# Kernel optimization log

Measured on AMD Instinct MI355X. Metric: run time of the kernel, lower is better.

The kernel has to match this reference:

```python
import jax, jax.numpy as jnp
import numpy as np

EPS = 1e-5
NEG = jnp.float32(-1e30)
SPP_LEVEL = 3
SPATIAL_SCALE = 0.125


def conv2d(x, w, b, pad):
    out = jax.lax.conv_general_dilated(x, w, (1, 1), [(pad, pad), (pad, pad)],
                                       dimension_numbers=('NCHW', 'OIHW', 'NCHW'))
    return out + b[None, :, None, None]


def bn2d(x, g, b):  # BatchNorm2d, training-mode batch stats (biased var), as in torch forward
    m = x.mean((0, 2, 3), keepdims=True)
    v = x.var((0, 2, 3), keepdims=True)
    return (x - m) * jax.lax.rsqrt(v + EPS) * g[None, :, None, None] + b[None, :, None, None]


def bn1d(x, g, b):
    m = x.mean(0)
    v = x.var(0)
    return (x - m) * jax.lax.rsqrt(v + EPS) * g + b


def maxpool2(x):
    return jax.lax.reduce_window(x, -jnp.inf, jax.lax.max, (1, 1, 2, 2), (1, 1, 2, 2), 'VALID')


def roi_spp(feat, roi):
    # feat: (B,C,Hf,Wf); roi: (R,5) int [im,x1,y1,x2,y2] in input-image coords.
    im = roi[:, 0].astype(jnp.int32)
    s = (roi[:, 1:].astype(jnp.float32) * SPATIAL_SCALE).astype(jnp.int32)  # trunc, coords >= 0
    c1, r1, c2, r2 = s[:, 0], s[:, 1], s[:, 2], s[:, 3]
    R = roi.shape[0]
    Hf, Wf = feat.shape[2], feat.shape[3]
    rows = jnp.arange(Hf)
    cols = jnp.arange(Wf)
    rmask = (rows[None, :] >= r1[:, None]) & (rows[None, :] <= r2[:, None])  # (R,Hf)
    w = c2 - c1 + 1
    froi = feat[im]  # (R,C,Hf,Wf)
    pieces = []
    for l in range(1, SPP_LEVEL + 1):  # adaptive_max_pool2d to (1,l) per level
        k = jnp.arange(l)
        lo = c1[:, None] + (k[None, :] * w[:, None]) // l
        hi = c1[:, None] + ((k[None, :] + 1) * w[:, None] + l - 1) // l - 1
        cmask = (cols[None, None, :] >= lo[:, :, None]) & (cols[None, None, :] <= hi[:, :, None])  # (R,l,Wf)
        mask = rmask[:, None, :, None] & cmask[:, :, None, :]  # (R,l,Hf,Wf)
        vals = jnp.where(mask[:, None], froi[:, :, None], NEG)  # (R,C,l,Hf,Wf)
        pieces.append(vals.max((-2, -1)).reshape(R, -1))  # channel-major flatten, like torch .view
    return jnp.concatenate(pieces, axis=1)  # (R, C*(1+2+3)) = (R, 3072)


def _forward(x, phocTensor, roi,
             c1w, c1b, g1, b1, c2w, c2b, g2, b2, c3w, c3b, g3, b3,
             c4w, c4b, g4, b4, c5w, c5b, g5, b5,
             f1w, f1b, g6, b6, f2w, f2b, g7, b7):
    out = jnp.pad(x, ((0, 0), (0, 0), (2, 2), (2, 2)), mode='edge')  # replicate pad
    out = maxpool2(jax.nn.relu(bn2d(conv2d(out, c1w, c1b, 0), g1, b1)))
    out = maxpool2(jax.nn.relu(bn2d(conv2d(out, c2w, c2b, 2), g2, b2)))
    out = jax.nn.relu(bn2d(conv2d(out, c3w, c3b, 1), g3, b3))
    out = maxpool2(jax.nn.relu(bn2d(conv2d(out, c4w, c4b, 1), g4, b4)))
    out = jax.nn.relu(bn2d(conv2d(out, c5w, c5b, 1), g5, b5))  # (B,512,6,16)
    out = roi_spp(out, roi)  # (R,3072)
    out = jax.nn.relu(bn1d(out @ f1w.T + f1b, g6, b6))
    out = jnp.concatenate([out, phocTensor], axis=1)  # (R, 2048+5853)
    out = jax.nn.relu(bn1d(out @ f2w.T + f2b, g7, b7))
    return out


def setup_inputs() -> dict:
    key = jax.random.key(0)
    ks = jax.random.split(key, 24)
    B, R = 64, 256
    x = jax.random.normal(ks[0], (B, 1, 48, 128), jnp.float32)
    # ROIs [im, x1, y1, x2, y2], guaranteed non-empty after /8 scaling
    im = jax.random.randint(ks[1], (R,), 0, B)
    x1 = jax.random.randint(ks[2], (R,), 0, 64)
    x2 = jnp.minimum(x1 + jax.random.randint(ks[3], (R,), 32, 64), 127)
    y1 = jax.random.randint(ks[4], (R,), 0, 16)
    y2 = jnp.minimum(y1 + jax.random.randint(ks[5], (R,), 16, 32), 47)
    roi = jnp.stack([im, x1, y1, x2, y2], axis=1).astype(jnp.int32)
    phocTensor = jax.random.uniform(ks[6], (R, 5853), jnp.float32)

    def he(k, shape):
        fan_in = int(np.prod(shape[1:]))
        return jax.random.normal(k, shape, jnp.float32) * np.sqrt(2.0 / fan_in).astype(np.float32)

    d = {'x': x, 'roi': roi, 'phocTensor': phocTensor}
    conv_shapes = [('c1', (64, 1, 5, 5)), ('c2', (128, 64, 5, 5)), ('c3', (256, 128, 3, 3)),
                   ('c4', (512, 256, 3, 3)), ('c5', (512, 512, 3, 3))]
    for i, (nm, sh) in enumerate(conv_shapes):
        d[nm + 'w'] = he(ks[7 + i], sh)
        d[nm + 'b'] = jnp.zeros((sh[0],), jnp.float32)
        d['g' + str(i + 1)] = jnp.ones((sh[0],), jnp.float32)
        d['b' + str(i + 1)] = jnp.zeros((sh[0],), jnp.float32)
    d['f1w'] = he(ks[12], (2048, 3072)); d['f1b'] = jnp.zeros((2048,), jnp.float32)
    d['g6'] = jnp.ones((2048,), jnp.float32); d['b6'] = jnp.zeros((2048,), jnp.float32)
    d['f2w'] = he(ks[13], (2048, 2048 + 5853)); d['f2b'] = jnp.zeros((2048,), jnp.float32)
    d['g7'] = jnp.ones((2048,), jnp.float32); d['b7'] = jnp.zeros((2048,), jnp.float32)
    return d


def reference(x, roi, phocTensor,
              c1w, c1b, g1, b1, c2w, c2b, g2, b2, c3w, c3b, g3, b3,
              c4w, c4b, g4, b4, c5w, c5b, g5, b5,
              f1w, f1b, g6, b6, f2w, f2b, g7, b7):
    return _forward(x, phocTensor, roi,
                    c1w, c1b, g1, b1, c2w, c2b, g2, b2, c3w, c3b, g3, b3,
                    c4w, c4b, g4, b4, c5w, c5b, g5, b5,
                    f1w, f1b, g6, b6, f2w, f2b, g7, b7)
```

## Files before the change

kernel.cpp:

```cpp
#include <hip/hip_runtime.h>
#include <hip/hip_bf16.h>


typedef __bf16 bf16;
using bf16x4 = __attribute__((ext_vector_type(4))) __bf16;
using bf16x8 = __attribute__((ext_vector_type(8))) __bf16;
using f32x4  = __attribute__((ext_vector_type(4))) float;

__device__ __forceinline__ void split2(float v, bf16& h, bf16& l) {
  bf16 hb = (bf16)v;
  h = hb;
  l = (bf16)(v - (float)hb);
}

__device__ __forceinline__ int iclamp(int v, int lo, int hi) {
  return v < lo ? lo : (v > hi ? hi : v);
}

__device__ __forceinline__ void gld_lds16(const bf16* g, void* lds) {
  __builtin_amdgcn_global_load_lds(
      (const __attribute__((address_space(1))) unsigned int*)g,
      (__attribute__((address_space(3))) unsigned int*)lds, 16, 0, 0);
}

__device__ __forceinline__ void wconv_tx(const float* __restrict__ w,
                                         bf16* __restrict__ oh_,
                                         bf16* __restrict__ ol_,
                                         int CI, int KS, int i, int total) {
  if (i >= total) return;
  int ci = i % CI; int t = i / CI; int kw = t % KS; t /= KS; int kh = t % KS; int co = t / KS;
  float v = w[(((size_t)co * CI + ci) * KS + kh) * KS + kw];
  bf16 h, l; split2(v, h, l);
  oh_[i] = h;
  if (ol_) ol_[i] = l;
}

__global__ __launch_bounds__(256) void prep_k(const float* __restrict__ c2w,
                                              const float* __restrict__ c3w,
                                              const float* __restrict__ c4w,
                                              const float* __restrict__ c5w,
                                              const float* __restrict__ f1w,
                                              const float* __restrict__ f2w,
                                              const float* __restrict__ phoc,
                                              bf16* __restrict__ Wc2h,
                                              bf16* __restrict__ Wc3h,
                                              bf16* __restrict__ Wc4h,
                                              bf16* __restrict__ Wc5h,
                                              bf16* __restrict__ Wc5l,
                                              bf16* __restrict__ Wf1,
                                              bf16* __restrict__ Wf2,
                                              bf16* __restrict__ cch,
                                              bf16* __restrict__ ccl) {
  int b = blockIdx.x;
  int tid = threadIdx.x;
  if (b < 800)  { wconv_tx(c2w, Wc2h, nullptr, 64, 5, b * 256 + tid, 204800); return; }
  b -= 800;
  if (b < 1152) { wconv_tx(c3w, Wc3h, nullptr, 128, 3, b * 256 + tid, 294912); return; }
  b -= 1152;
  if (b < 4608) { wconv_tx(c4w, Wc4h, nullptr, 256, 3, b * 256 + tid, 1179648); return; }
  b -= 4608;
  if (b < 9216) { wconv_tx(c5w, Wc5h, Wc5l, 512, 3, b * 256 + tid, 2359296); return; }
  b -= 9216;
  if (b < 6144) {
    int i = b * 256 + tid;
    const float4 v = *(const float4*)(f1w + (size_t)i * 4);
    bf16x4 o = { (bf16)v.x, (bf16)v.y, (bf16)v.z, (bf16)v.w };
    *(bf16x4*)(Wf1 + (size_t)i * 4) = o;
    return;
  }
  b -= 6144;
  if (b < 16384) {
    int i = b * 256 + tid;
    int k = (i & 2047) * 4, n = i >> 11;
    const float* xp = f2w + (size_t)n * 7901 + k;
    bf16x4 o;
#pragma unroll
    for (int j = 0; j < 4; j++) o[j] = (bf16)((k + j < 7901) ? xp[j] : 0.f);
    *(bf16x4*)(Wf2 + (size_t)n * 8192 + k) = o;
    return;
  }
  b -= 16384;
  {
    int i = b * 256 + tid;
    if (i >= 256 * 6144) return;
    int k = i % 6144, r = i / 6144;
    int col = 2048 + k;
    float v = (col < 7901) ? phoc[(size_t)r * 5853 + (col - 2048)] : 0.f;
    bf16 h, l; split2(v, h, l);
    cch[(size_t)r * 8192 + col] = h;
    ccl[(size_t)r * 8192 + col] = l;
  }
}

__global__ __launch_bounds__(256) void conv1_stats_k(const float* __restrict__ x,
                                                     const float* __restrict__ wt,
                                                     float* __restrict__ part) {
  int co0 = blockIdx.y * 8;
  float sums[8] = {0.f}, sqs[8] = {0.f};
  for (int r = 0; r < 16; r++) {
    int pix = blockIdx.x * 4096 + r * 256 + threadIdx.x;
    int w = pix & 127; int t = pix >> 7; int h = t % 48; int n = t / 48;
    const float* ip = x + (size_t)n * 48 * 128;
    int ihs[5], iws[5];
#pragma unroll
    for (int k = 0; k < 5; k++) {
      ihs[k] = iclamp(h + k - 2, 0, 47);
      iws[k] = iclamp(w + k - 2, 0, 127);
    }
    float win[25];
#pragma unroll
    for (int kh = 0; kh < 5; kh++)
#pragma unroll
      for (int kw = 0; kw < 5; kw++) win[kh * 5 + kw] = ip[ihs[kh] * 128 + iws[kw]];
#pragma unroll
    for (int j = 0; j < 8; j++) {
      const float* wp = wt + (size_t)(co0 + j) * 25;
      float acc = 0.f;
#pragma unroll
      for (int k = 0; k < 25; k++) acc += win[k] * wp[k];
      sums[j] += acc; sqs[j] += acc * acc;
    }
  }
  __shared__ float ls[256], lq[256];
  for (int j = 0; j < 8; j++) {
    ls[threadIdx.x] = sums[j]; lq[threadIdx.x] = sqs[j];
    __syncthreads();
    for (int o = 128; o > 0; o >>= 1) {
      if (threadIdx.x < o) { ls[threadIdx.x] += ls[threadIdx.x + o]; lq[threadIdx.x] += lq[threadIdx.x + o]; }
      __syncthreads();
    }
    if (threadIdx.x == 0) {
      int c = co0 + j;
      part[((size_t)c * 96 + blockIdx.x) * 2 + 0] = ls[0];
      part[((size_t)c * 96 + blockIdx.x) * 2 + 1] = lq[0];
    }
    __syncthreads();
  }
}

__global__ __launch_bounds__(256) void conv1_apply_k(const float* __restrict__ x,
                                                     const float* __restrict__ wt,
                                                     const float* __restrict__ scale,
                                                     const float* __restrict__ shift,
                                                     bf16* __restrict__ yh,
                                                     bf16* __restrict__ yl) {
  int i = blockIdx.x * 256 + threadIdx.x;
  if (i >= 64 * 28 * 68) return;
  int owp = i % 68; int t = i / 68; int ohp = t % 28; int n = t / 28;
  int co0 = blockIdx.y * 8;
  int oh = ohp - 2, ow = owp - 2;
  bf16x8 hv, lv;
#pragma unroll
  for (int j = 0; j < 8; j++) { hv[j] = (bf16)0.f; lv[j] = (bf16)0.f; }
  if (oh >= 0 && oh < 24 && ow >= 0 && ow < 64) {
    const float* ip = x + (size_t)n * 48 * 128;
    int shr[6], swc[6];
#pragma unroll
    for (int k = 0; k < 6; k++) {
      shr[k] = iclamp(2 * oh + k - 2, 0, 47);
      swc[k] = iclamp(2 * ow + k - 2, 0, 127);
    }
    float win[36];
#pragma unroll
    for (int r = 0; r < 6; r++)
#pragma unroll
      for (int c = 0; c < 6; c++) win[r * 6 + c] = ip[shr[r] * 128 + swc[c]];
#pragma unroll
    for (int j = 0; j < 8; j++) {
      const float* wp = wt + (size_t)(co0 + j) * 25;
      float sc = scale[co0 + j], sh = shift[co0 + j];
      float m = -1e30f;
#pragma unroll
      for (int dy = 0; dy < 2; dy++)
#pragma unroll
        for (int dx = 0; dx < 2; dx++) {
          float acc = 0.f;
#pragma unroll
          for (int kh = 0; kh < 5; kh++)
#pragma unroll
            for (int kw = 0; kw < 5; kw++)
              acc += win[(kh + dy) * 6 + kw + dx] * wp[kh * 5 + kw];
          m = fmaxf(m, acc * sc + sh);
        }
      float v = fmaxf(m, 0.f);
      bf16 h, l; split2(v, h, l);
      hv[j] = h; lv[j] = l;
    }
  }
  size_t o = (size_t)i * 64 + co0;
  *(bf16x8*)(yh + o) = hv;
  *(bf16x8*)(yl + o) = lv;
}

__global__ __launch_bounds__(256) void conv2_gemm_k(const bf16* __restrict__ Ahi,
                                                    const bf16* __restrict__ Bhi,
                                                    float* __restrict__ Cout,
                                                    float* __restrict__ part) {
  __shared__ bf16 Ash[416 * 64];
  __shared__ bf16 Bsh[128 * 64];
  __shared__ float red[2][128][8];
  const int t = threadIdx.x;
  const int lane = t & 63, w = t >> 6;
  const int m0 = blockIdx.x * 128;
  const int img = m0 / 1536;
  const int oh0 = (m0 % 1536) >> 6;
  const size_t abase = ((size_t)(img * 28 + oh0) * 68) * 64;

#pragma unroll
  for (int i = 0; i < 13; i++) {
    int f = i * 256 + t;
    int p = f >> 3; if (p > 407) p = 407;
    int s = f & 7;
    int ss = s ^ (p & 7);
    gld_lds16(Ahi + abase + (size_t)p * 64 + ss * 8,
              (char*)Ash + (size_t)(i * 256 + w * 64) * 16);
  }

  size_t boff[4];
#pragma unroll
  for (int i = 0; i < 4; i++) {
    int f = (i * 4 + w) * 64 + lane;
    int row = f >> 3, slot = f & 7;
    int ss = slot ^ (row & 7);
    boff[i] = (size_t)row * 1600 + ss * 8;
  }

  const int wrow = w >> 1, wcol = w & 1;
  const int kg = lane >> 4, l15 = lane & 15;
  int pixb[4];
#pragma unroll
  for (int q = 0; q < 4; q++) pixb[q] = wrow * 68 + q * 16 + l15;
  int brb[4], bmk[4];
#pragma unroll
  for (int q = 0; q < 4; q++) {
    int rb = wcol * 64 + q * 16 + l15;
    brb[q] = rb * 128; bmk[q] = rb & 7;
  }
  const char* Ashb = (const char*)Ash;
  const char* Bshb = (const char*)Bsh;

  f32x4 acc[4][4] = {};
  for (int kc = 0; kc < 25; ++kc) {
    const int kh = kc / 5, kw = kc % 5;
    const int kofs = kh * 68 + kw;
    const int k0 = kc * 64;
#pragma unroll
    for (int i = 0; i < 4; i++)
      gld_lds16(Bhi + boff[i] + k0, (char*)Bsh + (i * 4 + w) * 1024);
    __syncthreads();
#pragma unroll
    for (int ks = 0; ks < 2; ks++) {
      const int slot = ks * 4 + kg;
      bf16x8 ah[4], bh[4];
#pragma unroll
      for (int q = 0; q < 4; q++) {
        int pix = pixb[q] + kofs;
        ah[q] = *(const bf16x8*)(Ashb + pix * 128 + ((slot ^ (pix & 7)) << 4));
        bh[q] = *(const bf16x8*)(Bshb + brb[q] + ((slot ^ bmk[q]) << 4));
      }
#pragma unroll
      for (int mi = 0; mi < 4; mi++)
#pragma unroll
        for (int ni = 0; ni < 4; ni++)
          acc[mi][ni] = __builtin_amdgcn_mfma_f32_16x16x32_bf16(ah[mi], bh[ni], acc[mi][ni], 0, 0, 0);
    }
    __syncthreads();
  }

  const int crow0 = kg * 4, ccol = l15;
#pragma unroll
  for (int mi = 0; mi < 4; mi++) {
    int m = m0 + wrow * 64 + mi * 16 + crow0;
#pragma unroll
    for (int ni = 0; ni < 4; ni++) {
      int nn = wcol * 64 + ni * 16 + ccol;
      float* cp = Cout + (size_t)m * 128 + nn;
#pragma unroll
      for (int jj = 0; jj < 4; jj++) cp[(size_t)jj * 128] = acc[mi][ni][jj];
    }
  }
  const int contrib = kg * 2 + wrow;
#pragma unroll
  for (int ni = 0; ni < 4; ni++) {
    float s = 0.f, q = 0.f;
#pragma unroll
    for (int mi = 0; mi < 4; mi++)
#pragma unroll
      for (int jj = 0; jj < 4; jj++) {
        float v = acc[mi][ni][jj];
        s += v; q += v * v;
      }
    int coll = wcol * 64 + ni * 16 + ccol;
    red[0][coll][contrib] = s;
    red[1][coll][contrib] = q;
  }
  __syncthreads();
  if (t < 128) {
    float s = 0.f, q = 0.f;
#pragma unroll
    for (int j = 0; j < 8; j++) { s += red[0][t][j]; q += red[1][t][j]; }
    size_t c = t;
    part[(c * gridDim.x + blockIdx.x) * 2 + 0] = s;
    part[(c * gridDim.x + blockIdx.x) * 2 + 1] = q;
  }
}

template<int CI, int KS, int OH, int OW, int CO, bool ALO, bool BLO, int SPLIT>
__global__ __launch_bounds__(256) void conv_gemm_k(const bf16* __restrict__ Ahi,
                                                   const bf16* __restrict__ Alo,
                                                   const bf16* __restrict__ Bhi,
                                                   const bf16* __restrict__ Blo,
                                                   float* __restrict__ Cout,
                                                   float* __restrict__ part) {
  static_assert(CI % 64 == 0, "chunk must not straddle ci segments");
  constexpr int K = KS * KS * CI;
  constexpr int IWP = OW + KS - 1;
  constexpr int NCH = K / 64;
  static_assert(NCH % SPLIT == 0, "split must divide chunk count");
  constexpr int NCHS = NCH / SPLIT;
  constexpr int M = 64 * OH * OW;
  __shared__ bf16 Ash[128 * 64];
  __shared__ bf16 Asl[ALO ? 128 * 64 : 64];
  __shared__ bf16 Bsh[128 * 64];
  __shared__ bf16 Bsl[BLO ? 128 * 64 : 64];
  __shared__ float red[2][128][8];
  const int t = threadIdx.x;
  const int lane = t & 63, w = t >> 6;
  const int m0 = blockIdx.x * 128, n0 = blockIdx.y * 128;
  const int z = (SPLIT > 1) ? blockIdx.z : 0;

  int apix[4]; size_t boff[4];
#pragma unroll
  for (int i = 0; i < 4; i++) {
    int f = (i * 4 + w) * 64 + lane;
    int row = f >> 3, slot = f & 7;
    int ss = slot ^ (row & 7);
    int m = m0 + row;
    int n = m / (OH * OW); int rem = m % (OH * OW);
    int oh = rem / OW, ow_ = rem % OW;
    apix[i] = ((n * (OH + KS - 1) + oh) * IWP + ow_) * CI + ss * 8;
    boff[i] = (size_t)(n0 + row) * K + ss * 8;
  }

  const int wrow = w >> 1, wcol = w & 1;
  const int kg = lane >> 4, l15 = lane & 15;
  int arb[4], amk[4], brb[4], bmk[4];
#pragma unroll
  for (int q = 0; q < 4; q++) {
    int ra = wrow * 64 + q * 16 + l15;
    arb[q] = ra * 128; amk[q] = ra & 7;
    int rb = wcol * 64 + q * 16 + l15;
    brb[q] = rb * 128; bmk[q] = rb & 7;
  }
  const char* Ashb = (const char*)Ash;
  const char* Aslb = (const char*)Asl;
  const char* Bshb = (const char*)Bsh;
  const char* Bslb = (const char*)Bsl;

  f32x4 acc[4][4] = {};
  for (int kc = z * NCHS; kc < (z + 1) * NCHS; ++kc) {
    const int k0 = kc * 64;
    const int seg = k0 / CI;
    const int ci0 = k0 % CI;
    const int kh = seg / KS, kw = seg % KS;
    const int aoff = (kh * IWP + kw) * CI + ci0;
#pragma unroll
    for (int i = 0; i < 4; i++) {
      gld_lds16(Ahi + (size_t)apix[i] + aoff, (char*)Ash + (i * 4 + w) * 1024);
      if (ALO)
        gld_lds16(Alo + (size_t)apix[i] + aoff, (char*)Asl + (i * 4 + w) * 1024);
      gld_lds16(Bhi + boff[i] + k0,   (char*)Bsh + (i * 4 + w) * 1024);
      if (BLO)
        gld_lds16(Blo + boff[i] + k0, (char*)Bsl + (i * 4 + w) * 1024);
    }
    __syncthreads();
#pragma unroll
    for (int ks = 0; ks < 2; ks++) {
      const int slot = ks * 4 + kg;
      bf16x8 ah[4], bh[4];
#pragma unroll
      for (int q = 0; q < 4; q++) {
        ah[q] = *(const bf16x8*)(Ashb + arb[q] + ((slot ^ amk[q]) << 4));
        bh[q] = *(const bf16x8*)(Bshb + brb[q] + ((slot ^ bmk[q]) << 4));
      }
#pragma unroll
      for (int mi = 0; mi < 4; mi++)
#pragma unroll
        for (int ni = 0; ni < 4; ni++)
          acc[mi][ni] = __builtin_amdgcn_mfma_f32_16x16x32_bf16(ah[mi], bh[ni], acc[mi][ni], 0, 0, 0);
      if (ALO) {
        bf16x8 al[4];
#pragma unroll
        for (int q = 0; q < 4; q++)
          al[q] = *(const bf16x8*)(Aslb + arb[q] + ((slot ^ amk[q]) << 4));
#pragma unroll
        for (int mi = 0; mi < 4; mi++)
#pragma unroll
          for (int ni = 0; ni < 4; ni++)
            acc[mi][ni] = __builtin_amdgcn_mfma_f32_16x16x32_bf16(al[mi], bh[ni], acc[mi][ni], 0, 0, 0);
      }
      if (BLO) {
        bf16x8 bl[4];
#pragma unroll
        for (int q = 0; q < 4; q++)
          bl[q] = *(const bf16x8*)(Bslb + brb[q] + ((slot ^ bmk[q]) << 4));
#pragma unroll
        for (int mi = 0; mi < 4; mi++)
#pragma unroll
          for (int ni = 0; ni < 4; ni++)
            acc[mi][ni] = __builtin_amdgcn_mfma_f32_16x16x32_bf16(ah[mi], bl[ni], acc[mi][ni], 0, 0, 0);
      }
    }
    __syncthreads();
  }

  const int crow0 = kg * 4, ccol = l15;
  float* Cz = Cout + (size_t)z * M * CO;
#pragma unroll
  for (int mi = 0; mi < 4; mi++) {
    int m = m0 + wrow * 64 + mi * 16 + crow0;
#pragma unroll
    for (int ni = 0; ni < 4; ni++) {
      int nn = n0 + wcol * 64 + ni * 16 + ccol;
      float* cp = Cz + (size_t)m * CO + nn;
#pragma unroll
      for (int jj = 0; jj < 4; jj++) cp[(size_t)jj * CO] = acc[mi][ni][jj];
    }
  }
  if constexpr (SPLIT == 1) {
    const int contrib = kg * 2 + wrow;
#pragma unroll
    for (int ni = 0; ni < 4; ni++) {
      float s = 0.f, q = 0.f;
#pragma unroll
      for (int mi = 0; mi < 4; mi++)
#pragma unroll
        for (int jj = 0; jj < 4; jj++) {
          float v = acc[mi][ni][jj];
          s += v; q += v * v;
        }
      int coll = wcol * 64 + ni * 16 + ccol;
      red[0][coll][contrib] = s;
      red[1][coll][contrib] = q;
    }
    __syncthreads();
    if (t < 128) {
      float s = 0.f, q = 0.f;
#pragma unroll
      for (int j = 0; j < 8; j++) { s += red[0][t][j]; q += red[1][t][j]; }
      size_t c = n0 + t;
      part[(c * gridDim.x + blockIdx.x) * 2 + 0] = s;
      part[(c * gridDim.x + blockIdx.x) * 2 + 1] = q;
    }
  }
}

template<int M, int CO, int SPLIT, int NS>
__global__ __launch_bounds__(256) void reduce_bn_k(const float* __restrict__ Cp,
                                                   float* __restrict__ Cf,
                                                   float* __restrict__ part) {
  int c = blockIdx.x * 64 + (threadIdx.x & 63);
  int rl = threadIdx.x >> 6;
  constexpr int ROWS = M / NS;
  int r0 = blockIdx.y * ROWS;
  float sum = 0.f, sq = 0.f;
  for (int r = r0 + rl; r < r0 + ROWS; r += 4) {
    float v = 0.f;
#pragma unroll
    for (int s = 0; s < SPLIT; s++) v += Cp[(size_t)s * M * CO + (size_t)r * CO + c];
    Cf[(size_t)r * CO + c] = v;
    sum += v; sq += v * v;
  }
  __shared__ float ls[256], lq[256];
  ls[threadIdx.x] = sum; lq[threadIdx.x] = sq;
  __syncthreads();
  if (threadIdx.x < 64) {
    sum = ls[threadIdx.x] + ls[threadIdx.x + 64] + ls[threadIdx.x + 128] + ls[threadIdx.x + 192];
    sq  = lq[threadIdx.x] + lq[threadIdx.x + 64] + lq[threadIdx.x + 128] + lq[threadIdx.x + 192];
    part[((size_t)c * NS + blockIdx.y) * 2 + 0] = sum;
    part[((size_t)c * NS + blockIdx.y) * 2 + 1] = sq;
  }
}

__global__ __launch_bounds__(64) void bn_finalize(const float* __restrict__ part,
                                                  const float* __restrict__ g,
                                                  const float* __restrict__ b,
                                                  float* __restrict__ scale,
                                                  float* __restrict__ shift,
                                                  int S, float invCount) {
  int c = blockIdx.x;
  int lane = threadIdx.x;
  float sum = 0.f, sq = 0.f;
  for (int s = lane; s < S; s += 64) {
    sum += part[((size_t)c * S + s) * 2 + 0];
    sq  += part[((size_t)c * S + s) * 2 + 1];
  }
#pragma unroll
  for (int o = 32; o > 0; o >>= 1) {
    sum += __shfl_xor(sum, o);
    sq  += __shfl_xor(sq, o);
  }
  if (lane == 0) {
    float m = sum * invCount;
    float var = sq * invCount - m * m;
    float sc = g[c] * rsqrtf(var + 1e-5f);
    scale[c] = sc;
    shift[c] = b[c] - m * sc;
  }
}

template<int CO, int IH, int IW, bool POOL, int PADO>
__global__ __launch_bounds__(256) void bn_act_pad_k(const float* __restrict__ x,
                                                    const float* __restrict__ scale,
                                                    const float* __restrict__ shift,
                                                    bf16* __restrict__ yh,
                                                    bf16* __restrict__ yl) {
  constexpr int OH2 = POOL ? IH / 2 : IH, OW2 = POOL ? IW / 2 : IW;
  constexpr int OHP = OH2 + 2 * PADO, OWP = OW2 + 2 * PADO;
  constexpr int CO8 = CO / 8;
  int i = blockIdx.x * 256 + threadIdx.x;
  if (i >= 64 * OHP * OWP * CO8) return;
  int c8 = i % CO8; int t = i / CO8; int owp = t % OWP; t /= OWP; int ohp = t % OHP; int n = t / OHP;
  int c0 = c8 * 8;
  int oh = ohp - PADO, ow = owp - PADO;
  bf16x8 hv, lv;
#pragma unroll
  for (int j = 0; j < 8; j++) { hv[j] = (bf16)0.f; lv[j] = (bf16)0.f; }
  if (oh >= 0 && oh < OH2 && ow >= 0 && ow < OW2) {
    float sc[8], sh[8];
    *(f32x4*)(sc)     = *(const f32x4*)(scale + c0);
    *(f32x4*)(sc + 4) = *(const f32x4*)(scale + c0 + 4);
    *(f32x4*)(sh)     = *(const f32x4*)(shift + c0);
    *(f32x4*)(sh + 4) = *(const f32x4*)(shift + c0 + 4);
    float v[8];
    if (POOL) {
      const float* p = x + (((size_t)(n * IH) + oh * 2) * IW + ow * 2) * CO + c0;
      float ta[8], tb[8], tc[8], td[8];
      *(f32x4*)(ta) = *(const f32x4*)(p);            *(f32x4*)(ta + 4) = *(const f32x4*)(p + 4);
      *(f32x4*)(tb) = *(const f32x4*)(p + CO);       *(f32x4*)(tb + 4) = *(const f32x4*)(p + CO + 4);
      *(f32x4*)(tc) = *(const f32x4*)(p + (size_t)IW * CO);
      *(f32x4*)(tc + 4) = *(const f32x4*)(p + (size_t)IW * CO + 4);
      *(f32x4*)(td) = *(const f32x4*)(p + (size_t)(IW + 1) * CO);
      *(f32x4*)(td + 4) = *(const f32x4*)(p + (size_t)(IW + 1) * CO + 4);
#pragma unroll
      for (int j = 0; j < 8; j++) {
        float a = ta[j] * sc[j] + sh[j];
        float b2 = tb[j] * sc[j] + sh[j];
        float d = tc[j] * sc[j] + sh[j];
        float e = td[j] * sc[j] + sh[j];
        v[j] = fmaxf(fmaxf(a, b2), fmaxf(d, e));
      }
    } else {
      const float* p = x + (((size_t)(n * OH2) + oh) * OW2 + ow) * CO + c0;
      float ta[8];
      *(f32x4*)(ta) = *(const f32x4*)(p); *(f32x4*)(ta + 4) = *(const f32x4*)(p + 4);
#pragma unroll
      for (int j = 0; j < 8; j++) v[j] = ta[j] * sc[j] + sh[j];
    }
#pragma unroll
    for (int j = 0; j < 8; j++) {
      float vv = fmaxf(v[j], 0.f);
      bf16 h, l; split2(vv, h, l);
      hv[j] = h; lv[j] = l;
    }
  }
  size_t o = (size_t)i * 8;
  *(bf16x8*)(yh + o) = hv;
  *(bf16x8*)(yl + o) = lv;
}

__global__ __launch_bounds__(256) void spp_k(const float* __restrict__ feat,
                                             const float* __restrict__ scale,
                                             const float* __restrict__ shift,
                                             const int* __restrict__ roi,
                                             bf16* __restrict__ oh_,
                                             bf16* __restrict__ ol_) {
  int c = blockIdx.x * 256 + threadIdx.x;
  int r = blockIdx.y;
  const int* rp = roi + r * 5;
  int im = rp[0];
  int c1 = rp[1] >> 3, r1 = rp[2] >> 3, c2 = rp[3] >> 3, r2 = rp[4] >> 3;
  int w = c2 - c1 + 1;
  int lo[6], hi[6];
  int bi = 0;
#pragma unroll
  for (int l = 1; l <= 3; l++)
    for (int k = 0; k < l; k++) {
      lo[bi] = c1 + (k * w) / l;
      hi[bi] = c1 + ((k + 1) * w + l - 1) / l - 1;
      bi++;
    }
  float mx[6];
#pragma unroll
  for (int b = 0; b < 6; b++) mx[b] = -1e30f;
  float sc = scale[c], sh = shift[c];
  const float* fp = feat + (size_t)im * 96 * 512 + c;
  for (int row = r1; row <= r2; row++)
    for (int col = c1; col <= c2; col++) {
      float v = fp[(size_t)(row * 16 + col) * 512] * sc + sh;
#pragma unroll
      for (int b = 0; b < 6; b++)
        if (col >= lo[b] && col <= hi[b]) mx[b] = fmaxf(mx[b], v);
    }
  int idx[6] = {c, 512 + c * 2, 512 + c * 2 + 1, 1536 + c * 3, 1536 + c * 3 + 1, 1536 + c * 3 + 2};
#pragma unroll
  for (int b = 0; b < 6; b++) {
    float v = fmaxf(mx[b], 0.f);
    bf16 h, l; split2(v, h, l);
    oh_[(size_t)r * 3072 + idx[b]] = h;
    ol_[(size_t)r * 3072 + idx[b]] = l;
  }
}

__global__ __launch_bounds__(256) void bn1d_apply_cc_k(const float* __restrict__ x,
                                                       const float* __restrict__ scale,
                                                       const float* __restrict__ shift,
                                                       bf16* __restrict__ ch,
                                                       bf16* __restrict__ cl) {
  int i = blockIdx.x * 256 + threadIdx.x;
  if (i >= 256 * 256) return;
  int f8 = i & 255, r = i >> 8;
  int f0 = f8 * 8;
  float xv[8], sc[8], sh[8];
  *(f32x4*)(xv)     = *(const f32x4*)(x + (size_t)r * 2048 + f0);
  *(f32x4*)(xv + 4) = *(const f32x4*)(x + (size_t)r * 2048 + f0 + 4);
  *(f32x4*)(sc)     = *(const f32x4*)(scale + f0);
  *(f32x4*)(sc + 4) = *(const f32x4*)(scale + f0 + 4);
  *(f32x4*)(sh)     = *(const f32x4*)(shift + f0);
  *(f32x4*)(sh + 4) = *(const f32x4*)(shift + f0 + 4);
  bf16x8 hv, lv;
#pragma unroll
  for (int j = 0; j < 8; j++) {
    float v = fmaxf(xv[j] * sc[j] + sh[j], 0.f);
    bf16 h, l; split2(v, h, l);
    hv[j] = h; lv[j] = l;
  }
  *(bf16x8*)(ch + (size_t)r * 8192 + f0) = hv;
  *(bf16x8*)(cl + (size_t)r * 8192 + f0) = lv;
}

__global__ __launch_bounds__(256) void bn1d_apply_f32_k(const float* __restrict__ x,
                                                        const float* __restrict__ scale,
                                                        const float* __restrict__ shift,
                                                        float* __restrict__ y) {
  int i = blockIdx.x * 256 + threadIdx.x;
  if (i >= 256 * 512) return;
  int f4 = i & 511, r = i >> 9;
  int f0 = f4 * 4;
  f32x4 xv = *(const f32x4*)(x + (size_t)r * 2048 + f0);
  f32x4 sc = *(const f32x4*)(scale + f0);
  f32x4 sh = *(const f32x4*)(shift + f0);
  f32x4 o;
#pragma unroll
  for (int j = 0; j < 4; j++) o[j] = fmaxf(xv[j] * sc[j] + sh[j], 0.f);
  *(f32x4*)(y + (size_t)r * 2048 + f0) = o;
}

extern "C" void kernel_launch(void* const* d_in, const int* in_sizes, int n_in,
                              void* d_out, int out_size, void* d_ws, size_t ws_size,
                              hipStream_t stream) {
  (void)in_sizes; (void)n_in; (void)out_size; (void)ws_size;

  const float* x    = (const float*)d_in[0];
  const int*   roi  = (const int*)  d_in[1];
  const float* phoc = (const float*)d_in[2];
  const float* c1w  = (const float*)d_in[3];
  const float* g1   = (const float*)d_in[5];
  const float* b1   = (const float*)d_in[6];
  const float* c2w  = (const float*)d_in[7];
  const float* g2   = (const float*)d_in[9];
  const float* b2   = (const float*)d_in[10];
  const float* c3w  = (const float*)d_in[11];
  const float* g3   = (const float*)d_in[13];
  const float* b3   = (const float*)d_in[14];
  const float* c4w  = (const float*)d_in[15];
  const float* g4   = (const float*)d_in[17];
  const float* b4   = (const float*)d_in[18];
  const float* c5w  = (const float*)d_in[19];
  const float* g5   = (const float*)d_in[21];
  const float* b5   = (const float*)d_in[22];
  const float* f1w  = (const float*)d_in[23];
  const float* g6   = (const float*)d_in[25];
  const float* b6   = (const float*)d_in[26];
  const float* f2w  = (const float*)d_in[27];
  const float* g7   = (const float*)d_in[29];
  const float* b7   = (const float*)d_in[30];
  float* out = (float*)d_out;

  char* ws = (char*)d_ws;
  bf16*  Ahi  = (bf16*) (ws + 0x0200000);
  bf16*  Alo  = (bf16*) (ws + 0x1200000);
  float* C    = (float*)(ws + 0x2200000);
  float* C5F  = (float*)(ws + 0x4600000);
  bf16*  Wc2h = (bf16*) (ws + 0x5500000);
  bf16*  Wc3h = (bf16*) (ws + 0x5570000);
  bf16*  Wc4h = (bf16*) (ws + 0x5600000);
  bf16*  Wc5h = (bf16*) (ws + 0x5840000);
  bf16*  Wf1  = (bf16*) (ws + 0x5CC0000);
  bf16*  Wf2  = (bf16*) (ws + 0x68C0000);
  bf16*  Wc5l = (bf16*) (ws + 0x8C00000);
  bf16*  Shi  = (bf16*) (ws + 0x9080000);
  bf16*  Slo  = (bf16*) (ws + 0x9200000);
  float* G6   = (float*)(ws + 0x9380000);
  bf16*  CChi = (bf16*) (ws + 0x9580000);
  bf16*  CClo = (bf16*) (ws + 0x9980000);
  float* G7   = (float*)(ws + 0x9D80000);
  float* PART = (float*)(ws + 0x9F80000);
  float* SC   = (float*)(ws + 0xA040000);
  float* SH   = (float*)(ws + 0xA050000);

  prep_k<<<44448, 256, 0, stream>>>(c2w, c3w, c4w, c5w, f1w, f2w, phoc,
                                    Wc2h, Wc3h, Wc4h, Wc5h, Wc5l, Wf1, Wf2,
                                    CChi, CClo);

  conv1_stats_k<<<dim3(96, 8), 256, 0, stream>>>(x, c1w, PART);
  bn_finalize<<<64, 64, 0, stream>>>(PART, g1, b1, SC, SH, 96, 1.f / 393216.f);
  conv1_apply_k<<<dim3(476, 8), 256, 0, stream>>>(x, c1w, SC, SH, Ahi, Alo);

  conv2_gemm_k<<<768, 256, 0, stream>>>(Ahi, Wc2h, C, PART);
  bn_finalize<<<128, 64, 0, stream>>>(PART, g2, b2, SC, SH, 768, 1.f / 98304.f);
  bn_act_pad_k<128, 24, 64, true, 1><<<1904, 256, 0, stream>>>(C, SC, SH, Ahi, Alo);

  conv_gemm_k<128, 3, 12, 32, 256, true, false, 1><<<dim3(192, 2), 256, 0, stream>>>(Ahi, Alo, Wc3h, nullptr, C, PART);
  bn_finalize<<<256, 64, 0, stream>>>(PART, g3, b3, SC, SH, 192, 1.f / 24576.f);
  bn_act_pad_k<256, 12, 32, false, 1><<<3808, 256, 0, stream>>>(C, SC, SH, Ahi, Alo);

  conv_gemm_k<256, 3, 12, 32, 512, false, false, 1><<<dim3(192, 4), 256, 0, stream>>>(Ahi, Alo, Wc4h, nullptr, C, PART);
  bn_finalize<<<512, 64, 0, stream>>>(PART, g4, b4, SC, SH, 192, 1.f / 24576.f);
  bn_act_pad_k<512, 12, 32, true, 1><<<2304, 256, 0, stream>>>(C, SC, SH, Ahi, Alo);

  conv_gemm_k<512, 3, 6, 16, 512, true, true, 3><<<dim3(48, 4, 3), 256, 0, stream>>>(Ahi, Alo, Wc5h, Wc5l, C, nullptr);
  reduce_bn_k<6144, 512, 3, 16><<<dim3(8, 16), 256, 0, stream>>>(C, C5F, PART);
  bn_finalize<<<512, 64, 0, stream>>>(PART, g5, b5, SC, SH, 16, 1.f / 6144.f);

  spp_k<<<dim3(2, 256), 256, 0, stream>>>(C5F, SC, SH, roi, Shi, Slo);

  conv_gemm_k<3072, 1, 2, 2, 2048, true, false, 16><<<dim3(2, 16, 16), 256, 0, stream>>>(Shi, Slo, Wf1, nullptr, C, nullptr);
  reduce_bn_k<256, 2048, 16, 4><<<dim3(32, 4), 256, 0, stream>>>(C, G6, PART);
  bn_finalize<<<2048, 64, 0, stream>>>(PART, g6, b6, SC, SH, 4, 1.f / 256.f);
  bn1d_apply_cc_k<<<256, 256, 0, stream>>>(G6, SC, SH, CChi, CClo);

  conv_gemm_k<8192, 1, 2, 2, 2048, true, false, 16><<<dim3(2, 16, 16), 256, 0, stream>>>(CChi, CClo, Wf2, nullptr, C, nullptr);
  reduce_bn_k<256, 2048, 16, 4><<<dim3(32, 4), 256, 0, stream>>>(C, G7, PART);
  bn_finalize<<<2048, 64, 0, stream>>>(PART, g7, b7, SC, SH, 4, 1.f / 256.f);
  bn1d_apply_f32_k<<<512, 256, 0, stream>>>(G7, SC, SH, out);
}
```

Baseline: 590.1 us.

## Pre-pack weights into MFMA fragment layout and load B directly from global

Weights and FC activations are stored in a tiled layout where each 16-row by 64-k block matches the MFMA operand fragment, so each lane reads a contiguous 16-byte vector straight from global memory. The B-operand LDS staging and the per-chunk barriers are removed from the conv GEMMs, and a new fc_gemm_k reads A and B operands directly from global for the two FC layers. This cuts LDS traffic and synchronisation but relies on L1/L2 caching for operand reuse across waves. The prep, SPP and BN-apply kernels write in the packed layout to match.

```diff
diff --git a/kernel.cpp b/kernel.cpp
--- a/kernel.cpp
+++ b/kernel.cpp
@@ -17,6 +17,11 @@
   return v < lo ? lo : (v > hi ? hi : v);
 }
 
+__device__ __forceinline__ size_t pk_off(int row, int k, int Kd64) {
+  return ((size_t)(row >> 4) * Kd64 + (k >> 6)) * 1024 +
+         (size_t)(((k >> 5) & 1) * 512 + ((k >> 3) & 3) * 128 + ((row & 15) << 3) + (k & 7));
+}
+
 __device__ __forceinline__ void gld_lds16(const bf16* g, void* lds) {
   __builtin_amdgcn_global_load_lds(
       (const __attribute__((address_space(1))) unsigned int*)g,
@@ -26,13 +31,15 @@
 __device__ __forceinline__ void wconv_tx(const float* __restrict__ w,
                                          bf16* __restrict__ oh_,
                                          bf16* __restrict__ ol_,
-                                         int CI, int KS, int i, int total) {
+                                         int CI, int KS, int Kd64, int i, int total) {
   if (i >= total) return;
   int ci = i % CI; int t = i / CI; int kw = t % KS; t /= KS; int kh = t % KS; int co = t / KS;
+  int k = (kh * KS + kw) * CI + ci;
   float v = w[(((size_t)co * CI + ci) * KS + kh) * KS + kw];
   bf16 h, l; split2(v, h, l);
-  oh_[i] = h;
-  if (ol_) ol_[i] = l;
+  size_t o = pk_off(co, k, Kd64);
+  oh_[o] = h;
+  if (ol_) ol_[o] = l;
 }
 
 __global__ __launch_bounds__(256) void prep_k(const float* __restrict__ c2w,
@@ -53,30 +60,31 @@
                                               bf16* __restrict__ ccl) {
   int b = blockIdx.x;
   int tid = threadIdx.x;
-  if (b < 800)  { wconv_tx(c2w, Wc2h, nullptr, 64, 5, b * 256 + tid, 204800); return; }
+  if (b < 800)  { wconv_tx(c2w, Wc2h, nullptr, 64, 5, 25, b * 256 + tid, 204800); return; }
   b -= 800;
-  if (b < 1152) { wconv_tx(c3w, Wc3h, nullptr, 128, 3, b * 256 + tid, 294912); return; }
+  if (b < 1152) { wconv_tx(c3w, Wc3h, nullptr, 128, 3, 18, b * 256 + tid, 294912); return; }
   b -= 1152;
-  if (b < 4608) { wconv_tx(c4w, Wc4h, nullptr, 256, 3, b * 256 + tid, 1179648); return; }
+  if (b < 4608) { wconv_tx(c4w, Wc4h, nullptr, 256, 3, 36, b * 256 + tid, 1179648); return; }
   b -= 4608;
-  if (b < 9216) { wconv_tx(c5w, Wc5h, Wc5l, 512, 3, b * 256 + tid, 2359296); return; }
+  if (b < 9216) { wconv_tx(c5w, Wc5h, Wc5l, 512, 3, 72, b * 256 + tid, 2359296); return; }
   b -= 9216;
   if (b < 6144) {
     int i = b * 256 + tid;
-    const float4 v = *(const float4*)(f1w + (size_t)i * 4);
+    int k0 = (i % 768) * 4, n = i / 768;
+    const float4 v = *(const float4*)(f1w + (size_t)n * 3072 + k0);
     bf16x4 o = { (bf16)v.x, (bf16)v.y, (bf16)v.z, (bf16)v.w };
-    *(bf16x4*)(Wf1 + (size_t)i * 4) = o;
+    *(bf16x4*)(Wf1 + pk_off(n, k0, 48)) = o;
     return;
   }
   b -= 6144;
   if (b < 16384) {
     int i = b * 256 + tid;
-    int k = (i & 2047) * 4, n = i >> 11;
-    const float* xp = f2w + (size_t)n * 7901 + k;
+    int k0 = (i & 2047) * 4, n = i >> 11;
+    const float* xp = f2w + (size_t)n * 7901 + k0;
     bf16x4 o;
 #pragma unroll
-    for (int j = 0; j < 4; j++) o[j] = (bf16)((k + j < 7901) ? xp[j] : 0.f);
-    *(bf16x4*)(Wf2 + (size_t)n * 8192 + k) = o;
+    for (int j = 0; j < 4; j++) o[j] = (bf16)((k0 + j < 7901) ? xp[j] : 0.f);
+    *(bf16x4*)(Wf2 + pk_off(n, k0, 128)) = o;
     return;
   }
   b -= 16384;
@@ -87,8 +95,9 @@
     int col = 2048 + k;
     float v = (col < 7901) ? phoc[(size_t)r * 5853 + (col - 2048)] : 0.f;
     bf16 h, l; split2(v, h, l);
-    cch[(size_t)r * 8192 + col] = h;
-    ccl[(size_t)r * 8192 + col] = l;
+    size_t o = pk_off(r, col, 128);
+    cch[o] = h;
+    ccl[o] = l;
   }
 }
 
@@ -193,12 +202,11 @@
 }
 
 __global__ __launch_bounds__(256) void conv2_gemm_k(const bf16* __restrict__ Ahi,
-                                                    const bf16* __restrict__ Bhi,
+                                                    const bf16* __restrict__ Bhp,
                                                     float* __restrict__ Cout,
                                                     float* __restrict__ part) {
   __shared__ bf16 Ash[416 * 64];
-  __shared__ bf16 Bsh[128 * 64];
-  __shared__ float red[2][128][8];
+  __shared__ float red[2048];
   const int t = threadIdx.x;
   const int lane = t & 63, w = t >> 6;
   const int m0 = blockIdx.x * 128;
@@ -216,38 +224,24 @@
               (char*)Ash + (size_t)(i * 256 + w * 64) * 16);
   }
 
-  size_t boff[4];
-#pragma unroll
-  for (int i = 0; i < 4; i++) {
-    int f = (i * 4 + w) * 64 + lane;
-    int row = f >> 3, slot = f & 7;
-    int ss = slot ^ (row & 7);
-    boff[i] = (size_t)row * 1600 + ss * 8;
-  }
-
   const int wrow = w >> 1, wcol = w & 1;
   const int kg = lane >> 4, l15 = lane & 15;
   int pixb[4];
 #pragma unroll
   for (int q = 0; q < 4; q++) pixb[q] = wrow * 68 + q * 16 + l15;
-  int brb[4], bmk[4];
-#pragma unroll
-  for (int q = 0; q < 4; q++) {
-    int rb = wcol * 64 + q * 16 + l15;
-    brb[q] = rb * 128; bmk[q] = rb & 7;
-  }
+  size_t bb[4];
+#pragma unroll
+  for (int q = 0; q < 4; q++)
+    bb[q] = (size_t)(wcol * 4 + q) * 25 * 1024 + (size_t)lane * 8;
   const char* Ashb = (const char*)Ash;
-  const char* Bshb = (const char*)Bsh;
+
+  __syncthreads();
 
   f32x4 acc[4][4] = {};
   for (int kc = 0; kc < 25; ++kc) {
     const int kh = kc / 5, kw = kc % 5;
     const int kofs = kh * 68 + kw;
-    const int k0 = kc * 64;
-#pragma unroll
-    for (int i = 0; i < 4; i++)
-      gld_lds16(Bhi + boff[i] + k0, (char*)Bsh + (i * 4 + w) * 1024);
-    __syncthreads();
+    const size_t bco = (size_t)kc * 1024;
 #pragma unroll
     for (int ks = 0; ks < 2; ks++) {
       const int slot = ks * 4 + kg;
@@ -256,7 +250,7 @@
       for (int q = 0; q < 4; q++) {
         int pix = pixb[q] + kofs;
         ah[q] = *(const bf16x8*)(Ashb + pix * 128 + ((slot ^ (pix & 7)) << 4));
-        bh[q] = *(const bf16x8*)(Bshb + brb[q] + ((slot ^ bmk[q]) << 4));
+        bh[q] = *(const bf16x8*)(Bhp + bb[q] + bco + ks * 512);
       }
 #pragma unroll
       for (int mi = 0; mi < 4; mi++)
@@ -264,7 +258,6 @@
         for (int ni = 0; ni < 4; ni++)
           acc[mi][ni] = __builtin_amdgcn_mfma_f32_16x16x32_bf16(ah[mi], bh[ni], acc[mi][ni], 0, 0, 0);
     }
-    __syncthreads();
   }
 
   const int crow0 = kg * 4, ccol = l15;
@@ -291,14 +284,14 @@
         s += v; q += v * v;
       }
     int coll = wcol * 64 + ni * 16 + ccol;
-    red[0][coll][contrib] = s;
-    red[1][coll][contrib] = q;
+    red[coll * 8 + contrib] = s;
+    red[1024 + coll * 8 + contrib] = q;
   }
   __syncthreads();
   if (t < 128) {
     float s = 0.f, q = 0.f;
 #pragma unroll
-    for (int j = 0; j < 8; j++) { s += red[0][t][j]; q += red[1][t][j]; }
+    for (int j = 0; j < 8; j++) { s += red[t * 8 + j]; q += red[1024 + t * 8 + j]; }
     size_t c = t;
     part[(c * gridDim.x + blockIdx.x) * 2 + 0] = s;
     part[(c * gridDim.x + blockIdx.x) * 2 + 1] = q;
@@ -308,8 +301,8 @@
 template<int CI, int KS, int OH, int OW, int CO, bool ALO, bool BLO, int SPLIT>
 __global__ __launch_bounds__(256) void conv_gemm_k(const bf16* __restrict__ Ahi,
                                                    const bf16* __restrict__ Alo,
-                                                   const bf16* __restrict__ Bhi,
-                                                   const bf16* __restrict__ Blo,
+                                                   const bf16* __restrict__ Bhp,
+                                                   const bf16* __restrict__ Blp,
                                                    float* __restrict__ Cout,
                                                    float* __restrict__ part) {
   static_assert(CI % 64 == 0, "chunk must not straddle ci segments");
@@ -320,16 +313,14 @@
   constexpr int NCHS = NCH / SPLIT;
   constexpr int M = 64 * OH * OW;
   __shared__ bf16 Ash[128 * 64];
-  __shared__ bf16 Asl[ALO ? 128 * 64 : 64];
-  __shared__ bf16 Bsh[128 * 64];
-  __shared__ bf16 Bsl[BLO ? 128 * 64 : 64];
-  __shared__ float red[2][128][8];
+  __shared__ bf16 Asl[ALO ? 128 * 64 : 8];
+  __shared__ float red[SPLIT == 1 ? 2048 : 8];
   const int t = threadIdx.x;
   const int lane = t & 63, w = t >> 6;
   const int m0 = blockIdx.x * 128, n0 = blockIdx.y * 128;
   const int z = (SPLIT > 1) ? blockIdx.z : 0;
 
-  int apix[4]; size_t boff[4];
+  int apix[4];
 #pragma unroll
   for (int i = 0; i < 4; i++) {
     int f = (i * 4 + w) * 64 + lane;
@@ -339,23 +330,21 @@
     int n = m / (OH * OW); int rem = m % (OH * OW);
     int oh = rem / OW, ow_ = rem % OW;
     apix[i] = ((n * (OH + KS - 1) + oh) * IWP + ow_) * CI + ss * 8;
-    boff[i] = (size_t)(n0 + row) * K + ss * 8;
   }
 
   const int wrow = w >> 1, wcol = w & 1;
   const int kg = lane >> 4, l15 = lane & 15;
-  int arb[4], amk[4], brb[4], bmk[4];
+  int arb[4], amk[4];
+  size_t bb[4];
 #pragma unroll
   for (int q = 0; q < 4; q++) {
     int ra = wrow * 64 + q * 16 + l15;
     arb[q] = ra * 128; amk[q] = ra & 7;
-    int rb = wcol * 64 + q * 16 + l15;
-    brb[q] = rb * 128; bmk[q] = rb & 7;
+    int rbB = (n0 >> 4) + wcol * 4 + q;
+    bb[q] = (size_t)rbB * NCH * 1024 + (size_t)lane * 8;
   }
   const char* Ashb = (const char*)Ash;
   const char* Aslb = (const char*)Asl;
-  const char* Bshb = (const char*)Bsh;
-  const char* Bslb = (const char*)Bsl;
 
   f32x4 acc[4][4] = {};
   for (int kc = z * NCHS; kc < (z + 1) * NCHS; ++kc) {
@@ -369,11 +358,9 @@
       gld_lds16(Ahi + (size_t)apix[i] + aoff, (char*)Ash + (i * 4 + w) * 1024);
       if (ALO)
         gld_lds16(Alo + (size_t)apix[i] + aoff, (char*)Asl + (i * 4 + w) * 1024);
-      gld_lds16(Bhi + boff[i] + k0,   (char*)Bsh + (i * 4 + w) * 1024);
-      if (BLO)
-        gld_lds16(Blo + boff[i] + k0, (char*)Bsl + (i * 4 + w) * 1024);
     }
     __syncthreads();
+    const size_t bco = (size_t)kc * 1024;
 #pragma unroll
     for (int ks = 0; ks < 2; ks++) {
       const int slot = ks * 4 + kg;
@@ -381,7 +368,7 @@
 #pragma unroll
       for (int q = 0; q < 4; q++) {
         ah[q] = *(const bf16x8*)(Ashb + arb[q] + ((slot ^ amk[q]) << 4));
-        bh[q] = *(const bf16x8*)(Bshb + brb[q] + ((slot ^ bmk[q]) << 4));
+        bh[q] = *(const bf16x8*)(Bhp + bb[q] + bco + ks * 512);
       }
 #pragma unroll
       for (int mi = 0; mi < 4; mi++)
@@ -403,7 +390,7 @@
         bf16x8 bl[4];
 #pragma unroll
         for (int q = 0; q < 4; q++)
-          bl[q] = *(const bf16x8*)(Bslb + brb[q] + ((slot ^ bmk[q]) << 4));
+          bl[q] = *(const bf16x8*)(Blp + bb[q] + bco + ks * 512);
 #pragma unroll
         for (int mi = 0; mi < 4; mi++)
 #pragma unroll
@@ -440,17 +427,82 @@
           s += v; q += v * v;
         }
       int coll = wcol * 64 + ni * 16 + ccol;
-      red[0][coll][contrib] = s;
-      red[1][coll][contrib] = q;
+      red[coll * 8 + contrib] = s;
+      red[1024 + coll * 8 + contrib] = q;
     }
     __syncthreads();
     if (t < 128) {
       float s = 0.f, q = 0.f;
 #pragma unroll
-      for (int j = 0; j < 8; j++) { s += red[0][t][j]; q += red[1][t][j]; }
+      for (int j = 0; j < 8; j++) { s += red[t * 8 + j]; q += red[1024 + t * 8 + j]; }
       size_t c = n0 + t;
       part[(c * gridDim.x + blockIdx.x) * 2 + 0] = s;
       part[(c * gridDim.x + blockIdx.x) * 2 + 1] = q;
+    }
+  }
+}
+
+template<int K, int SPLIT>
+__global__ __launch_bounds__(256) void fc_gemm_k(const bf16* __restrict__ Ahp,
+                                                 const bf16* __restrict__ Alp,
+                                                 const bf16* __restrict__ Bhp,
+                                                 float* __restrict__ Cout) {
+  constexpr int Kd64 = K / 64;
+  constexpr int NCHS = Kd64 / SPLIT;
+  constexpr int M = 256, N = 2048;
+  const int t = threadIdx.x;
+  const int lane = t & 63, w = t >> 6;
+  const int m0 = blockIdx.x * 128, n0 = blockIdx.y * 128;
+  const int z = blockIdx.z;
+  const int wrow = w >> 1, wcol = w & 1;
+  const int kg = lane >> 4, l15 = lane & 15;
+
+  size_t ab[4], bb[4];
+#pragma unroll
+  for (int q = 0; q < 4; q++) {
+    int rbA = (m0 >> 4) + wrow * 4 + q;
+    ab[q] = (size_t)rbA * Kd64 * 1024 + (size_t)lane * 8;
+    int rbB = (n0 >> 4) + wcol * 4 + q;
+    bb[q] = (size_t)rbB * Kd64 * 1024 + (size_t)lane * 8;
+  }
+
+  f32x4 acc[4][4] = {};
+  for (int kc = z * NCHS; kc < (z + 1) * NCHS; ++kc) {
+    const size_t bco = (size_t)kc * 1024;
+#pragma unroll
+    for (int ks = 0; ks < 2; ks++) {
+      const size_t soff = bco + ks * 512;
+      bf16x8 ah[4], al[4], bh[4];
+#pragma unroll
+      for (int q = 0; q < 4; q++) {
+        ah[q] = *(const bf16x8*)(Ahp + ab[q] + soff);
+        al[q] = *(const bf16x8*)(Alp + ab[q] + soff);
+        bh[q] = *(const bf16x8*)(Bhp + bb[q] + soff);
+      }
+#pragma unroll
+      for (int mi = 0; mi < 4; mi++)
+#pragma unroll
+        for (int ni = 0; ni < 4; ni++)
+          acc[mi][ni] = __builtin_amdgcn_mfma_f32_16x16x32_bf16(ah[mi], bh[ni], acc[mi][ni], 0, 0, 0);
+#pragma unroll
+      for (int mi = 0; mi < 4; mi++)
+#pragma unroll
+        for (int ni = 0; ni < 4; ni++)
+          acc[mi][ni] = __builtin_amdgcn_mfma_f32_16x16x32_bf16(al[mi], bh[ni], acc[mi][ni], 0, 0, 0);
+    }
+  }
+
+  const int crow0 = kg * 4, ccol = l15;
+  float* Cz = Cout + (size_t)z * M * N;
+#pragma unroll
+  for (int mi = 0; mi < 4; mi++) {
+    int m = m0 + wrow * 64 + mi * 16 + crow0;
+#pragma unroll
+    for (int ni = 0; ni < 4; ni++) {
+      int nn = n0 + wcol * 64 + ni * 16 + ccol;
+      float* cp = Cz + (size_t)m * N + nn;
+#pragma unroll
+      for (int jj = 0; jj < 4; jj++) cp[(size_t)jj * N] = acc[mi][ni][jj];
     }
   }
 }
@@ -607,8 +659,9 @@
   for (int b = 0; b < 6; b++) {
     float v = fmaxf(mx[b], 0.f);
     bf16 h, l; split2(v, h, l);
-    oh_[(size_t)r * 3072 + idx[b]] = h;
-    ol_[(size_t)r * 3072 + idx[b]] = l;
+    size_t o = pk_off(r, idx[b], 48);
+    oh_[o] = h;
+    ol_[o] = l;
   }
 }
 
@@ -635,8 +688,9 @@
     bf16 h, l; split2(v, h, l);
     hv[j] = h; lv[j] = l;
   }
-  *(bf16x8*)(ch + (size_t)r * 8192 + f0) = hv;
-  *(bf16x8*)(cl + (size_t)r * 8192 + f0) = lv;
+  size_t o = pk_off(r, f0, 128);
+  *(bf16x8*)(ch + o) = hv;
+  *(bf16x8*)(cl + o) = lv;
 }
 
 __global__ __launch_bounds__(256) void bn1d_apply_f32_k(const float* __restrict__ x,
@@ -735,12 +789,12 @@
 
   spp_k<<<dim3(2, 256), 256, 0, stream>>>(C5F, SC, SH, roi, Shi, Slo);
 
-  conv_gemm_k<3072, 1, 2, 2, 2048, true, false, 16><<<dim3(2, 16, 16), 256, 0, stream>>>(Shi, Slo, Wf1, nullptr, C, nullptr);
+  fc_gemm_k<3072, 16><<<dim3(2, 16, 16), 256, 0, stream>>>(Shi, Slo, Wf1, C);
   reduce_bn_k<256, 2048, 16, 4><<<dim3(32, 4), 256, 0, stream>>>(C, G6, PART);
   bn_finalize<<<2048, 64, 0, stream>>>(PART, g6, b6, SC, SH, 4, 1.f / 256.f);
   bn1d_apply_cc_k<<<256, 256, 0, stream>>>(G6, SC, SH, CChi, CClo);
 
-  conv_gemm_k<8192, 1, 2, 2, 2048, true, false, 16><<<dim3(2, 16, 16), 256, 0, stream>>>(CChi, CClo, Wf2, nullptr, C, nullptr);
+  fc_gemm_k<8192, 16><<<dim3(2, 16, 16), 256, 0, stream>>>(CChi, CClo, Wf2, C);
   reduce_bn_k<256, 2048, 16, 4><<<dim3(32, 4), 256, 0, stream>>>(C, G7, PART);
   bn_finalize<<<2048, 64, 0, stream>>>(PART, g7, b7, SC, SH, 4, 1.f / 256.f);
   bn1d_apply_f32_k<<<512, 256, 0, stream>>>(G7, SC, SH, out);
```

Result: slower. 616.0 us (+4.4%).
